# Kernel tuning notes

Measured on AMD Instinct MI355X. Metric: run time of the kernel, lower is better.

## Reference

```python
import jax, jax.numpy as jnp
import numpy as np

FEATURES = 4096
BATCH = 2048


def setup_inputs() -> dict:
    key = jax.random.key(0)
    kx, kk = jax.random.split(key)
    x = jax.random.normal(kx, (BATCH, FEATURES), dtype=jnp.float32)
    kernel = jax.random.normal(kk, (FEATURES,), dtype=jnp.float32)
    return {"x": x, "kernel": kernel}


def reference(x, kernel):
    n = kernel.shape[0]
    i = jnp.arange(n)[:, None]   # [n,1]
    j = jnp.arange(n)[None, :]   # [1,n]
    idx = i - j                   # Toeplitz offsets
    # W[i,j] = kernel[i-j] if i>=j else 0  (causal lower-triangular Toeplitz)
    W = jnp.where(idx >= 0, kernel[jnp.clip(idx, 0, n - 1)], 0.0)
    # out[b,i] = sum_{j<=i} x[b,j] * kernel[i-j]  == x @ W.T
    return x @ W.T
```

## Files before the change

### kernel.cpp

```cpp
#include <hip/hip_runtime.h>
#include <hip/hip_bf16.h>


typedef unsigned short u16;
typedef __attribute__((ext_vector_type(8))) short  bf16x8;
typedef __attribute__((ext_vector_type(8))) unsigned short u16x8;
typedef __attribute__((ext_vector_type(4))) float  f32x4;

#define KDIM 4096
#define NDIM 4096
#define MDIM 2048
#define KREV_STRIDE 4608
#define KREV_BYTES  (8 * KREV_STRIDE * 2)
#define BSTRIDE 520

static __device__ inline u16 f2bf(float f) {
  unsigned u = __builtin_bit_cast(unsigned, f);
  unsigned r = u + 0x7FFFu + ((u >> 16) & 1u);
  return (u16)(r >> 16);
}

static __device__ inline void async_copy16(const void* g, void* l) {
  __builtin_amdgcn_global_load_lds((const __attribute__((address_space(1))) void*)g,
                                   (__attribute__((address_space(3))) void*)l,
                                   16, 0, 0);
}

__global__ __launch_bounds__(256) void prep(const float* __restrict__ x,
                                            const float* __restrict__ kern,
                                            u16* __restrict__ xb,
                                            u16* __restrict__ krevs,
                                            int conv_blocks) {
  int kb = (int)blockIdx.x - conv_blocks;
  if (kb >= 0) {
    int u = kb * 256 + threadIdx.x;
    for (int a = 0; a < 8; ++a) {
      int t = u + a - 8;
      u16 v = 0;
      if (t >= 0 && t <= 4095) v = f2bf(kern[4095 - t]);
      krevs[a * KREV_STRIDE + u] = v;
    }
  } else {
    size_t i = ((size_t)blockIdx.x * 256 + threadIdx.x) * 8;
    const f32x4* p = (const f32x4*)(x + i);
    f32x4 v0 = p[0], v1 = p[1];
    u16x8 r;
    r[0] = f2bf(v0[0]); r[1] = f2bf(v0[1]); r[2] = f2bf(v0[2]); r[3] = f2bf(v0[3]);
    r[4] = f2bf(v1[0]); r[5] = f2bf(v1[1]); r[6] = f2bf(v1[2]); r[7] = f2bf(v1[3]);
    *(u16x8*)(xb + i) = r;
  }
}

template <bool CONV>
__global__ __launch_bounds__(256, 2) void toeplitz_gemm(const void* __restrict__ Av,
                                                        const u16* __restrict__ krevs,
                                                        float* __restrict__ out) {
  __shared__ u16 A_lds[128 * 64];
  __shared__ u16 B_lds[8 * BSTRIDE];

  const int tid  = threadIdx.x;
  const int w    = tid >> 6;
  const int lane = tid & 63;
  const int lane16 = lane & 15;
  const int quad   = lane >> 4;
  const int wm = w >> 1;
  const int wn = w & 1;

  const int b    = (int)blockIdx.x;
  const int rank = (b < 256) ? b : 511 - (b & 255);
  const int ct   = 31 - (rank >> 4);
  const int n0   = ct * 128;
  const int m0   = (rank & 15) * 128;
  const int W    = 3968 - n0;

  int boff[4];
  for (int fn = 0; fn < 4; ++fn) {
    int n_g = n0 + wn * 64 + fn * 16 + lane16;
    int s0  = 4095 - n_g + quad * 8;
    int a   = s0 & 7;
    int ub  = s0 - a + 8 - W;
    boff[fn] = a * BSTRIDE + ub;
  }

  f32x4 acc[4][4] = {};
  const int nk = 2 * ct + 2;

  const int srow8  = lane >> 3;
  const int ssrc   = ((lane & 7) ^ srow8) * 8;

  for (int ks = 0; ks < nk; ++ks) {
    const int k0 = ks * 64;
    __syncthreads();
    if ((ks & 3) == 0) {
      for (int cc = 0; cc < 2; ++cc) {
        int c = cc * 4 + w;
        async_copy16(krevs + c * KREV_STRIDE + W + k0 + (lane << 3),
                     &B_lds[c * BSTRIDE]);
      }
    }
    if constexpr (CONV) {
      const float* x = (const float*)Av;
      int row  = tid & 127;
      int colq = tid >> 7;
      for (int lc = 0; lc < 4; ++lc) {
        int l = colq * 4 + lc;
        int p = l ^ (row & 7);
        const f32x4* px = (const f32x4*)(x + (size_t)(m0 + row) * KDIM + k0 + l * 8);
        f32x4 v0 = px[0], v1 = px[1];
        u16x8 r;
        r[0]=f2bf(v0[0]); r[1]=f2bf(v0[1]); r[2]=f2bf(v0[2]); r[3]=f2bf(v0[3]);
        r[4]=f2bf(v1[0]); r[5]=f2bf(v1[1]); r[6]=f2bf(v1[2]); r[7]=f2bf(v1[3]);
        *(u16x8*)(&A_lds[row * 64 + p * 8]) = r;
      }
    } else {
      const u16* xb = (const u16*)Av;
      for (int c = 0; c < 4; ++c) {
        int g   = c * 4 + w;
        int row = g * 8 + srow8;
        async_copy16(xb + (size_t)(m0 + row) * KDIM + k0 + ssrc,
                     &A_lds[g * 512]);
      }
    }
    __syncthreads();

    const int ksl = (ks & 3) * 64;
    for (int kk = 0; kk < 2; ++kk) {
      bf16x8 af[4];
      const int p = (kk * 4 + quad) ^ (lane16 & 7);
      for (int fm = 0; fm < 4; ++fm) {
        int row = wm * 64 + fm * 16 + lane16;
        af[fm] = *(const bf16x8*)(&A_lds[row * 64 + p * 8]);
      }
      bf16x8 bf[4];
      for (int fn = 0; fn < 4; ++fn)
        bf[fn] = *(const bf16x8*)(&B_lds[boff[fn] + ksl + kk * 32]);
      for (int fm = 0; fm < 4; ++fm)
        for (int fn = 0; fn < 4; ++fn)
          acc[fm][fn] = __builtin_amdgcn_mfma_f32_16x16x32_bf16(af[fm], bf[fn], acc[fm][fn], 0, 0, 0);
    }
  }

  for (int fm = 0; fm < 4; ++fm) {
    int row_base = m0 + wm * 64 + fm * 16 + quad * 4;
    for (int fn = 0; fn < 4; ++fn) {
      int col = n0 + wn * 64 + fn * 16 + lane16;
      for (int r = 0; r < 4; ++r)
        out[(size_t)(row_base + r) * NDIM + col] = acc[fm][fn][r];
    }
  }
}

extern "C" void kernel_launch(void* const* d_in, const int* in_sizes, int n_in,
                              void* d_out, int out_size, void* d_ws, size_t ws_size,
                              hipStream_t stream) {
  const float* x    = (const float*)d_in[0];
  const float* kern = (const float*)d_in[1];
  float* out = (float*)d_out;

  u16* krevs = (u16*)d_ws;
  u16* xb    = (u16*)((char*)d_ws + KREV_BYTES);
  const size_t need_fast = (size_t)KREV_BYTES + (size_t)MDIM * KDIM * 2;

  if (ws_size >= need_fast) {
    prep<<<4096 + 18, 256, 0, stream>>>(x, kern, xb, krevs, 4096);
    toeplitz_gemm<false><<<512, 256, 0, stream>>>(xb, krevs, out);
  } else {
    prep<<<18, 256, 0, stream>>>(x, kern, xb, krevs, 0);
    toeplitz_gemm<true><<<512, 256, 0, stream>>>(x, krevs, out);
  }
}
```

Measured before the change: 137.8 us.

## Double-buffer A and B LDS tiles to prefetch the next k-step during MFMA

```diff
diff --git a/kernel.cpp b/kernel.cpp
--- a/kernel.cpp
+++ b/kernel.cpp
@@ -52,11 +52,11 @@
 }
 
 template <bool CONV>
-__global__ __launch_bounds__(256, 2) void toeplitz_gemm(const void* __restrict__ Av,
+__global__ __launch_bounds__(256, 3) void toeplitz_gemm(const void* __restrict__ Av,
                                                         const u16* __restrict__ krevs,
                                                         float* __restrict__ out) {
-  __shared__ u16 A_lds[128 * 64];
-  __shared__ u16 B_lds[8 * BSTRIDE];
+  __shared__ u16 A_lds[2][128 * 64];
+  __shared__ u16 B_lds[2][8 * BSTRIDE];
 
   const int tid  = threadIdx.x;
   const int w    = tid >> 6;
@@ -85,55 +85,69 @@
   f32x4 acc[4][4] = {};
   const int nk = 2 * ct + 2;
 
-  const int srow8  = lane >> 3;
-  const int ssrc   = ((lane & 7) ^ srow8) * 8;
+  const int srow8 = lane >> 3;
+  const int ssrc  = ((lane & 7) ^ srow8) * 8;
 
-  for (int ks = 0; ks < nk; ++ks) {
-    const int k0 = ks * 64;
-    __syncthreads();
-    if ((ks & 3) == 0) {
-      for (int cc = 0; cc < 2; ++cc) {
-        int c = cc * 4 + w;
-        async_copy16(krevs + c * KREV_STRIDE + W + k0 + (lane << 3),
-                     &B_lds[c * BSTRIDE]);
-      }
-    }
+  const u16* xb = (const u16*)Av;
+  const float* xf = (const float*)Av;
+
+  auto stageA = [&](int ks) {
+    const int buf = ks & 1;
+    const int k0  = ks * 64;
     if constexpr (CONV) {
-      const float* x = (const float*)Av;
       int row  = tid & 127;
       int colq = tid >> 7;
       for (int lc = 0; lc < 4; ++lc) {
         int l = colq * 4 + lc;
         int p = l ^ (row & 7);
-        const f32x4* px = (const f32x4*)(x + (size_t)(m0 + row) * KDIM + k0 + l * 8);
+        const f32x4* px = (const f32x4*)(xf + (size_t)(m0 + row) * KDIM + k0 + l * 8);
         f32x4 v0 = px[0], v1 = px[1];
         u16x8 r;
         r[0]=f2bf(v0[0]); r[1]=f2bf(v0[1]); r[2]=f2bf(v0[2]); r[3]=f2bf(v0[3]);
         r[4]=f2bf(v1[0]); r[5]=f2bf(v1[1]); r[6]=f2bf(v1[2]); r[7]=f2bf(v1[3]);
-        *(u16x8*)(&A_lds[row * 64 + p * 8]) = r;
+        *(u16x8*)(&A_lds[buf][row * 64 + p * 8]) = r;
       }
     } else {
-      const u16* xb = (const u16*)Av;
       for (int c = 0; c < 4; ++c) {
         int g   = c * 4 + w;
         int row = g * 8 + srow8;
         async_copy16(xb + (size_t)(m0 + row) * KDIM + k0 + ssrc,
-                     &A_lds[g * 512]);
+                     &A_lds[buf][g * 512]);
       }
     }
+  };
+  auto stageB = [&](int ch) {
+    const int bb = ch & 1;
+    for (int cc = 0; cc < 2; ++cc) {
+      int c = cc * 4 + w;
+      async_copy16(krevs + c * KREV_STRIDE + W + ch * 256 + (lane << 3),
+                   &B_lds[bb][c * BSTRIDE]);
+    }
+  };
+
+  stageB(0);
+  stageA(0);
+
+  for (int ks = 0; ks < nk; ++ks) {
     __syncthreads();
-
+    const int nxt = ks + 1;
+    if (nxt < nk) {
+      stageA(nxt);
+      if ((nxt & 3) == 0) stageB(nxt >> 2);
+    }
+    const u16* Ab = A_lds[ks & 1];
+    const u16* Bb = B_lds[(ks >> 2) & 1];
     const int ksl = (ks & 3) * 64;
     for (int kk = 0; kk < 2; ++kk) {
       bf16x8 af[4];
       const int p = (kk * 4 + quad) ^ (lane16 & 7);
       for (int fm = 0; fm < 4; ++fm) {
         int row = wm * 64 + fm * 16 + lane16;
-        af[fm] = *(const bf16x8*)(&A_lds[row * 64 + p * 8]);
+        af[fm] = *(const bf16x8*)(&Ab[row * 64 + p * 8]);
       }
       bf16x8 bf[4];
       for (int fn = 0; fn < 4; ++fn)
-        bf[fn] = *(const bf16x8*)(&B_lds[boff[fn] + ksl + kk * 32]);
+        bf[fn] = *(const bf16x8*)(&Bb[boff[fn] + ksl + kk * 32]);
       for (int fm = 0; fm < 4; ++fm)
         for (int fn = 0; fn < 4; ++fn)
           acc[fm][fn] = __builtin_amdgcn_mfma_f32_16x16x32_bf16(af[fm], bf[fn], acc[fm][fn], 0, 0, 0);
```

Result: no change. 135.9 us (-1.4%).
